# Kernel optimization log

Measured on AMD Instinct MI355X. Metric: run time of the kernel, lower is better.

Reference implementation:

```python
import jax, jax.numpy as jnp
import numpy as np
from jax.scipy.special import gammaln

T_STEPS, N_GRID, NMUL = 730, 10000, 2
NEARZERO = 1e-5
LENF = 15  # unit-hydrograph length used by UH_gamma routing
STAT_NAMES = ["parFC", "parK0", "parK1", "parK2", "parLP", "parPERC", "parUZL",
              "parTT", "parCFMAX", "parCFR", "parCWH", "parC", "parRT", "parAC"]
BOUNDS = {"parBETA": (1.0, 6.0), "parFC": (50.0, 1000.0), "parK0": (0.05, 0.9),
          "parK1": (0.01, 0.5), "parK2": (0.001, 0.2), "parLP": (0.2, 1.0),
          "parPERC": (0.0, 10.0), "parUZL": (0.0, 100.0), "parTT": (-2.5, 2.5),
          "parCFMAX": (0.5, 10.0), "parCFR": (0.0, 0.1), "parCWH": (0.0, 0.2),
          "parBETAET": (0.3, 5.0), "parC": (0.0, 1.0), "parRT": (0.0, 20.0),
          "parAC": (0.0, 2500.0)}
ROUT_A = (0.0, 2.9)
ROUT_B = (0.0, 6.5)


def _scale(p, lo, hi):
    # change_param_range: affine map of [0,1]-normalized params to physical bounds
    return p * (hi - lo) + lo


def setup_inputs() -> dict:
    key = jax.random.key(0)
    ks = jax.random.split(key, 7)
    prcp = jax.random.uniform(ks[0], (T_STEPS, N_GRID)) * 10.0          # mm/day
    tmean = jax.random.uniform(ks[1], (T_STEPS, N_GRID)) * 30.0 - 10.0  # deg C, spans parTT range
    pet = jax.random.uniform(ks[2], (T_STEPS, N_GRID)) * 5.0            # mm/day
    x_phy = jnp.stack([prcp, tmean, pet], axis=-1).astype(jnp.float32)
    ac_all = jax.random.uniform(ks[3], (N_GRID,)) * 2500.0              # drainage area per unit basin
    elev_all = jax.random.uniform(ks[4], (N_GRID,)) * 3000.0            # elevation
    params_dy = jax.random.uniform(ks[5], (T_STEPS, N_GRID, 2 * NMUL))  # dynamic: parBETA, parBETAET
    params_stat = jax.random.uniform(ks[6], (N_GRID, 14 * NMUL + 2))    # 14 static phy + 2 routing
    return {"x_phy": x_phy, "ac_all": ac_all, "elev_all": elev_all,
            "params_dy": params_dy, "params_stat": params_stat}


def _forward(x_phy, ac_all, elev_all, params_dy, params_stat):
    T, G, _ = x_phy.shape
    P, Tair, PET = x_phy[..., 0], x_phy[..., 1], x_phy[..., 2]
    # expand forcing to nmul parameter components
    Pm = jnp.broadcast_to(P[..., None], (T, G, NMUL))
    Tm = jnp.broadcast_to(Tair[..., None], (T, G, NMUL))
    PETm = jnp.broadcast_to(PET[..., None], (T, G, NMUL))
    Ac = jnp.broadcast_to(ac_all[:, None], (G, NMUL))

    # dynamic (per-timestep) params; dy_drop=0.0 -> bernoulli drop mask is all zeros,
    # so the dynamic values are used directly at every step
    dy = params_dy.reshape(T, G, 2, NMUL)
    parBETA = _scale(dy[:, :, 0], *BOUNDS["parBETA"])
    parBETAET = _scale(dy[:, :, 1], *BOUNDS["parBETAET"])

    # static params: [G, 14, NMUL]
    stat = params_stat[:, :14 * NMUL].reshape(G, 14, NMUL)
    sp = {n: _scale(stat[:, i], *BOUNDS[n]) for i, n in enumerate(STAT_NAMES)}
    rout_a = _scale(params_stat[:, 14 * NMUL], *ROUT_A)
    rout_b = _scale(params_stat[:, 14 * NMUL + 1], *ROUT_B)

    def step(carry, xt):
        SNOWPACK, MELTWATER, SM, SUZ, SLZ = carry
        Pt, Tt, PETt, beta, betaet = xt
        rain_mask = (Tt >= sp["parTT"]).astype(Pt.dtype)
        RAIN = Pt * rain_mask
        SNOW = Pt * (1.0 - rain_mask)
        # --- snow bucket ---
        SNOWPACK = SNOWPACK + SNOW
        melt = jnp.maximum(sp["parCFMAX"] * (Tt - sp["parTT"]), 0.0)
        melt = jnp.minimum(melt, SNOWPACK)
        MELTWATER = MELTWATER + melt
        SNOWPACK = SNOWPACK - melt
        refreeze = jnp.maximum(sp["parCFR"] * sp["parCFMAX"] * (sp["parTT"] - Tt), 0.0)
        refreeze = jnp.minimum(refreeze, MELTWATER)
        SNOWPACK = SNOWPACK + refreeze
        MELTWATER = MELTWATER - refreeze
        tosoil = jnp.maximum(MELTWATER - sp["parCWH"] * SNOWPACK, 0.0)
        MELTWATER = MELTWATER - tosoil
        # --- soil bucket ---
        soil_wetness = jnp.clip((SM / sp["parFC"]) ** beta, 0.0, 1.0)
        recharge = (RAIN + tosoil) * soil_wetness
        SM = SM + RAIN + tosoil - recharge
        excess = jnp.maximum(SM - sp["parFC"], 0.0)
        SM = SM - excess
        evapfactor = jnp.clip(SM / (sp["parLP"] * sp["parFC"]), 0.0, 1.0) ** betaet
        ETact = jnp.minimum(SM, PETt * evapfactor)
        SM = jnp.maximum(SM - ETact, NEARZERO)
        # capillary rise from lower groundwater zone (parC)
        capillary = jnp.minimum(SLZ, sp["parC"] * SLZ * (1.0 - jnp.minimum(SM / sp["parFC"], 1.0)))
        SM = jnp.maximum(SM + capillary, NEARZERO)
        SLZ = jnp.maximum(SLZ - capillary, NEARZERO)
        # --- groundwater buckets ---
        SUZ = SUZ + recharge + excess
        PERC = jnp.minimum(SUZ, sp["parPERC"])
        SUZ = SUZ - PERC
        Q0 = sp["parK0"] * jnp.maximum(SUZ - sp["parUZL"], 0.0)
        SUZ = SUZ - Q0
        Q1 = sp["parK1"] * SUZ
        SUZ = SUZ - Q1
        SLZ = SLZ + PERC
        # HBV 2.0 regional groundwater loss (area-dependent via parRT / parAC; reconstructed)
        gw_loss = jnp.minimum(SLZ, sp["parRT"] * jnp.clip(1.0 - Ac / (sp["parAC"] + NEARZERO), 0.0, 1.0))
        SLZ = SLZ - gw_loss
        Q2 = sp["parK2"] * SLZ
        SLZ = SLZ - Q2
        Qt = Q0 + Q1 + Q2
        return (SNOWPACK, MELTWATER, SM, SUZ, SLZ), Qt

    init = tuple(jnp.full((G, NMUL), 1e-3, dtype=x_phy.dtype) for _ in range(5))
    _, Qsimmu = jax.lax.scan(step, init, (Pm, Tm, PETm, parBETA, parBETAET))
    Qsim = Qsimmu.mean(-1)  # [T, G]; muwts=None -> uniform average over nmul components

    # --- gamma unit-hydrograph routing (UH_gamma + causal UH_conv) ---
    a = jnp.maximum(rout_a, 0.0) + 0.1       # [G]
    theta = jnp.maximum(rout_b, 0.0) + 0.5   # [G]
    t = jnp.arange(LENF, dtype=Qsim.dtype) + 0.5  # [LENF]
    w = (jnp.exp(-gammaln(a))[None, :] * theta[None, :] ** (-a[None, :])
         * t[:, None] ** (a[None, :] - 1.0) * jnp.exp(-t[:, None] / theta[None, :]))
    w = w / w.sum(0)  # [LENF, G], normalized UH weights
    # causal grouped conv: flow[t] = sum_k w[k] * Qsim[t-k]
    Qpad = jnp.pad(Qsim, ((LENF - 1, 0), (0, 0)))
    flow = jnp.zeros_like(Qsim)
    for k in range(LENF):  # fixed, small tap count
        flow = flow + w[k][None, :] * Qpad[LENF - 1 - k: LENF - 1 - k + T]
    return flow[..., None]  # [T, G, 1] routed streamflow


def reference(x_phy, ac_all, elev_all, params_dy, params_stat):
    return _forward(x_phy, ac_all, elev_all, params_dy, params_stat)
```

## Files before the change

### kernel.cpp

```cpp
#include <hip/hip_runtime.h>


#define TS 730
#define NG 10000
#define CH 15
#define NCHUNK 49
#define XSTRIDE (NG * 3)
#define DSTRIDE (NG * 4)

#define AS1 __attribute__((address_space(1)))
#define AS3 __attribute__((address_space(3)))
#define WAIT_VMCNT(n) __builtin_amdgcn_s_waitcnt(((n) & 15) | 0x70 | 0xF00 | (((n) >> 4) << 14))
#define WAIT_LGKM0    __builtin_amdgcn_s_waitcnt(0xC07F)

__device__ __forceinline__ void gload16(const float* g, float* l) {
    __builtin_amdgcn_global_load_lds((const AS1 void*)g, (AS3 void*)l, 16, 0, 0);
}
__device__ __forceinline__ float powpos(float x, float b) {
    return __builtin_amdgcn_exp2f(b * __builtin_amdgcn_logf(x));
}

__global__ __launch_bounds__(64, 1) void hbv_fused(
    const float* __restrict__ x_phy,
    const float* __restrict__ ac_all,
    const float* __restrict__ params_dy,
    const float* __restrict__ params_stat,
    float* __restrict__ out)
{
    __shared__ float xls0[1536], xls1[1536];
    __shared__ float dls0[2048], dls1[2048];

    const int lane = threadIdx.x & 63;
    const int m    = lane >> 5;
    const int cell = lane & 31;
    const int g0   = blockIdx.x * 32;
    const int g    = g0 + cell;
    const int gl   = g < NG ? g : NG - 1;
    const int g0r  = (g0 <= NG - 32) ? g0 : NG - 32;
    const int co   = cell + (g0 - g0r);
    const int cl   = co < 31 ? co : 31;

    const float* ps = params_stat + (size_t)gl * 30;
    const float FC    = ps[0  + m] * 950.f   + 50.f;
    const float K0    = ps[2  + m] * 0.85f   + 0.05f;
    const float K1    = ps[4  + m] * 0.49f   + 0.01f;
    const float K2    = ps[6  + m] * 0.199f  + 0.001f;
    const float LP    = ps[8  + m] * 0.8f    + 0.2f;
    const float PERCp = ps[10 + m] * 10.f;
    const float UZL   = ps[12 + m] * 100.f;
    const float TTp   = ps[14 + m] * 5.f     - 2.5f;
    const float CFMAX = ps[16 + m] * 9.5f    + 0.5f;
    const float CFR   = ps[18 + m] * 0.1f;
    const float CWH   = ps[20 + m] * 0.2f;
    const float Cc    = ps[22 + m];
    const float RT    = ps[24 + m] * 20.f;
    const float ACp   = ps[26 + m] * 2500.f;
    const float ra    = ps[28] * 2.9f;
    const float rb    = ps[29] * 6.5f;

    const float Acv     = ac_all[gl];
    const float invFC   = 1.f / FC;
    const float invLPFC = 1.f / (LP * FC);
    const float CFRC    = CFR * CFMAX;
    const float gwcap   = RT * fminf(fmaxf(1.f - Acv / (ACp + 1e-5f), 0.f), 1.f);

    const float a     = fmaxf(ra, 0.f) + 0.1f;
    const float th    = fmaxf(rb, 0.f) + 0.5f;
    const float am1   = a - 1.f;
    const float nl2e  = 1.44269504f / th;
    float w[CH];
    float wsum = 0.f;
#pragma unroll
    for (int k = 0; k < CH; ++k) {
        const float tk = (float)k + 0.5f;
        const float v  = __builtin_amdgcn_exp2f(am1 * __builtin_amdgcn_logf(tk) - tk * nl2e);
        w[k] = v; wsum += v;
    }
    const float wn = 0.5f / wsum;
#pragma unroll
    for (int k = 0; k < CH; ++k) w[k] *= wn;

    int offx[6], offd[8];
#pragma unroll
    for (int i = 0; i < 6; ++i) {
        int idx = i * 64 + lane;
        idx = idx < 360 ? idx : 359;
        const int row = idx / 24;
        const int col = idx - row * 24;
        offx[i] = row * XSTRIDE + col * 4;
    }
#pragma unroll
    for (int i = 0; i < 8; ++i) {
        int idx = i * 64 + lane;
        idx = idx < 480 ? idx : 479;
        const int row = idx >> 5;
        const int col = idx & 31;
        offd[i] = row * DSTRIDE + col * 4;
    }
    const float* xbase = x_phy     + (size_t)g0r * 3;
    const float* dbase = params_dy + (size_t)g0r * 4;

    auto issue = [&](int cc, float* xl, float* dl) {
        if (cc == NCHUNK - 1) {
#pragma unroll
            for (int i = 0; i < 6; ++i) {
                int idx = i * 64 + lane; idx = idx < 360 ? idx : 359;
                const int row = idx / 24, col = idx - row * 24;
                int t = cc * CH + row; t = t < TS ? t : TS - 1;
                gload16(xbase + (size_t)t * XSTRIDE + col * 4, xl + i * 256);
            }
#pragma unroll
            for (int i = 0; i < 8; ++i) {
                int idx = i * 64 + lane; idx = idx < 480 ? idx : 479;
                const int row = idx >> 5, col = idx & 31;
                int t = cc * CH + row; t = t < TS ? t : TS - 1;
                gload16(dbase + (size_t)t * DSTRIDE + col * 4, dl + i * 256);
            }
        } else {
            const float* xp = xbase + (size_t)cc * CH * XSTRIDE;
            const float* dp = dbase + (size_t)cc * CH * DSTRIDE;
#pragma unroll
            for (int i = 0; i < 6; ++i) gload16(xp + offx[i], xl + i * 256);
#pragma unroll
            for (int i = 0; i < 8; ++i) gload16(dp + offd[i], dl + i * 256);
        }
    };

    float SP = 1e-3f, MW = 1e-3f, SM = 1e-3f, SUZ = 1e-3f, SLZ = 1e-3f;
    float facc[CH];
#pragma unroll
    for (int k = 0; k < CH; ++k) facc[k] = 0.f;

    const bool doStore = (g < NG) && (lane < 32);

    auto chunk = [&](int c, const float* xl, const float* dl) {
        float ofl[CH];
        float Pc = xl[cl * 3 + 0], Tc = xl[cl * 3 + 1], Ec = xl[cl * 3 + 2];
        float4 dvc = *(const float4*)&dl[cl * 4];
#pragma unroll
        for (int j = 0; j < CH; ++j) {
            float Pn, Tn, En; float4 dvn;
            if (j < CH - 1) {
                Pn  = xl[(j + 1) * 96 + cl * 3 + 0];
                Tn  = xl[(j + 1) * 96 + cl * 3 + 1];
                En  = xl[(j + 1) * 96 + cl * 3 + 2];
                dvn = *(const float4*)&dl[(j + 1) * 128 + cl * 4];
            }
            const float Pt = Pc, Tt = Tc, PETt = Ec;
            const float beta   = (m ? dvc.y : dvc.x) * 5.f  + 1.f;
            const float betaet = (m ? dvc.w : dvc.z) * 4.7f + 0.3f;

            const float rain = (Tt >= TTp) ? Pt : 0.f;
            SP += Pt - rain;
            const float melt = fminf(fmaxf(CFMAX * (Tt - TTp), 0.f), SP);
            MW += melt; SP -= melt;
            const float refr = fminf(fmaxf(CFRC * (TTp - Tt), 0.f), MW);
            SP += refr; MW -= refr;
            const float tosoil = fmaxf(MW - CWH * SP, 0.f);
            MW -= tosoil;

            const float sw   = fminf(powpos(SM * invFC, beta), 1.f);
            const float rts  = rain + tosoil;
            SM = fmaf(rts, 1.f - sw, SM);
            const float exc = fmaxf(SM - FC, 0.f);
            SM = fminf(SM, FC);
            const float ef = powpos(fminf(SM * invLPFC, 1.f), betaet);
            const float ET = fminf(SM, PETt * ef);
            SM = fmaxf(SM - ET, 1e-5f);
            const float cap = Cc * SLZ * (1.f - fminf(SM * invFC, 1.f));
            SM  = fmaxf(SM + cap, 1e-5f);
            SLZ = fmaxf(SLZ - cap, 1e-5f);

            SUZ += rts * sw + exc;
            const float perc = fminf(SUZ, PERCp);
            SUZ -= perc;
            const float Q0 = K0 * fmaxf(SUZ - UZL, 0.f);
            SUZ -= Q0;
            const float Q1 = K1 * SUZ;
            SUZ -= Q1;
            SLZ += perc;
            const float gw = fminf(SLZ, gwcap);
            SLZ -= gw;
            const float Q2 = K2 * SLZ;
            SLZ -= Q2;
            const float Qt = Q0 + Q1 + Q2;

#pragma unroll
            for (int k = 0; k < CH; ++k)
                facc[(j + k) % CH] = fmaf(w[k], Qt, facc[(j + k) % CH]);
            ofl[j]  = facc[j];
            facc[j] = 0.f;

            Pc = Pn; Tc = Tn; Ec = En; dvc = dvn;
        }
        float prt[CH];
#pragma unroll
        for (int j = 0; j < CH; ++j) prt[j] = __shfl_xor(ofl[j], 32);
        if (doStore) {
            float* op = out + (size_t)c * CH * NG + g;
            const int tb = c * CH;
#pragma unroll
            for (int j = 0; j < CH; ++j)
                if (tb + j < TS) op[(size_t)j * NG] = ofl[j] + prt[j];
        }
    };

    issue(0, xls0, dls0);
    issue(1, xls1, dls1);

    for (int cp = 0; cp < 24; ++cp) {
        const int c0 = 2 * cp;
        WAIT_VMCNT(14);
        chunk(c0, xls0, dls0);
        WAIT_LGKM0;
        issue(c0 + 2, xls0, dls0);
        WAIT_VMCNT(14);
        chunk(c0 + 1, xls1, dls1);
        WAIT_LGKM0;
        if (cp < 23) issue(c0 + 3, xls1, dls1);
    }
    WAIT_VMCNT(14);
    chunk(48, xls0, dls0);
}

extern "C" void kernel_launch(void* const* d_in, const int* in_sizes, int n_in,
                              void* d_out, int out_size, void* d_ws, size_t ws_size,
                              hipStream_t stream) {
    const float* x_phy = (const float*)d_in[0];
    const float* ac    = (const float*)d_in[1];
    const float* pdy   = (const float*)d_in[3];
    const float* pst   = (const float*)d_in[4];
    float* out = (float*)d_out;

    const int grid = (NG + 31) / 32;
    hbv_fused<<<grid, 64, 0, stream>>>(x_phy, ac, pdy, pst, out);
}
```

Before: 323.1 us.

## Stage chunk from LDS into registers and issue next prefetch before compute

Each 15-step chunk's forcing and dynamic parameters are now read from LDS into registers up front. The global-to-LDS prefetch for chunk c+2 is issued right after that read instead of after the chunk's compute, which gives the loads more time to land. The vmcnt wait thresholds are raised so the in-flight loads and stores can overlap the compute. Some clamps also become fmed3, and the groundwater step becomes a single fmax, which shortens the serial dependence chain a little but costs more registers.

```diff
diff --git a/kernel.cpp b/kernel.cpp
--- a/kernel.cpp
+++ b/kernel.cpp
@@ -18,6 +18,9 @@
 }
 __device__ __forceinline__ float powpos(float x, float b) {
     return __builtin_amdgcn_exp2f(b * __builtin_amdgcn_logf(x));
+}
+__device__ __forceinline__ float med3(float x, float lo, float hi) {
+    return __builtin_amdgcn_fmed3f(x, lo, hi);
 }
 
 __global__ __launch_bounds__(64, 1) void hbv_fused(
@@ -133,34 +136,38 @@
 
     const bool doStore = (g < NG) && (lane < 32);
 
-    auto chunk = [&](int c, const float* xl, const float* dl) {
+    auto chunkR = [&](int c, float* xl, float* dl) {
+        float xP[CH], xT[CH], xE[CH];
+        float4 dv[CH];
+#pragma unroll
+        for (int j = 0; j < CH; ++j) {
+            xP[j] = xl[j * 96 + cl * 3 + 0];
+            xT[j] = xl[j * 96 + cl * 3 + 1];
+            xE[j] = xl[j * 96 + cl * 3 + 2];
+            dv[j] = *(const float4*)&dl[j * 128 + cl * 4];
+        }
+        WAIT_LGKM0;
+        __builtin_amdgcn_sched_barrier(0);
+        const int cn = c + 2;
+        if (cn < NCHUNK) issue(cn, xl, dl);
         float ofl[CH];
-        float Pc = xl[cl * 3 + 0], Tc = xl[cl * 3 + 1], Ec = xl[cl * 3 + 2];
-        float4 dvc = *(const float4*)&dl[cl * 4];
 #pragma unroll
         for (int j = 0; j < CH; ++j) {
-            float Pn, Tn, En; float4 dvn;
-            if (j < CH - 1) {
-                Pn  = xl[(j + 1) * 96 + cl * 3 + 0];
-                Tn  = xl[(j + 1) * 96 + cl * 3 + 1];
-                En  = xl[(j + 1) * 96 + cl * 3 + 2];
-                dvn = *(const float4*)&dl[(j + 1) * 128 + cl * 4];
-            }
-            const float Pt = Pc, Tt = Tc, PETt = Ec;
-            const float beta   = (m ? dvc.y : dvc.x) * 5.f  + 1.f;
-            const float betaet = (m ? dvc.w : dvc.z) * 4.7f + 0.3f;
+            const float Pt = xP[j], Tt = xT[j], PETt = xE[j];
+            const float beta   = (m ? dv[j].y : dv[j].x) * 5.f  + 1.f;
+            const float betaet = (m ? dv[j].w : dv[j].z) * 4.7f + 0.3f;
 
             const float rain = (Tt >= TTp) ? Pt : 0.f;
             SP += Pt - rain;
-            const float melt = fminf(fmaxf(CFMAX * (Tt - TTp), 0.f), SP);
+            const float melt = med3(CFMAX * (Tt - TTp), 0.f, SP);
             MW += melt; SP -= melt;
-            const float refr = fminf(fmaxf(CFRC * (TTp - Tt), 0.f), MW);
+            const float refr = med3(CFRC * (TTp - Tt), 0.f, MW);
             SP += refr; MW -= refr;
             const float tosoil = fmaxf(MW - CWH * SP, 0.f);
             MW -= tosoil;
 
-            const float sw   = fminf(powpos(SM * invFC, beta), 1.f);
-            const float rts  = rain + tosoil;
+            const float sw  = fminf(powpos(SM * invFC, beta), 1.f);
+            const float rts = rain + tosoil;
             SM = fmaf(rts, 1.f - sw, SM);
             const float exc = fmaxf(SM - FC, 0.f);
             SM = fminf(SM, FC);
@@ -179,8 +186,7 @@
             const float Q1 = K1 * SUZ;
             SUZ -= Q1;
             SLZ += perc;
-            const float gw = fminf(SLZ, gwcap);
-            SLZ -= gw;
+            SLZ = fmaxf(SLZ - gwcap, 0.f);
             const float Q2 = K2 * SLZ;
             SLZ -= Q2;
             const float Qt = Q0 + Q1 + Q2;
@@ -190,19 +196,18 @@
                 facc[(j + k) % CH] = fmaf(w[k], Qt, facc[(j + k) % CH]);
             ofl[j]  = facc[j];
             facc[j] = 0.f;
-
-            Pc = Pn; Tc = Tn; Ec = En; dvc = dvn;
         }
         float prt[CH];
 #pragma unroll
-        for (int j = 0; j < CH; ++j) prt[j] = __shfl_xor(ofl[j], 32);
+        for (int jj = 0; jj < CH; ++jj) prt[jj] = __shfl_xor(ofl[jj], 32);
         if (doStore) {
             float* op = out + (size_t)c * CH * NG + g;
             const int tb = c * CH;
 #pragma unroll
-            for (int j = 0; j < CH; ++j)
-                if (tb + j < TS) op[(size_t)j * NG] = ofl[j] + prt[j];
-        }
+            for (int jj = 0; jj < CH; ++jj)
+                if (tb + jj < TS) op[(size_t)jj * NG] = ofl[jj] + prt[jj];
+        }
+        __builtin_amdgcn_sched_barrier(0);
     };
 
     issue(0, xls0, dls0);
@@ -210,17 +215,13 @@
 
     for (int cp = 0; cp < 24; ++cp) {
         const int c0 = 2 * cp;
-        WAIT_VMCNT(14);
-        chunk(c0, xls0, dls0);
-        WAIT_LGKM0;
-        issue(c0 + 2, xls0, dls0);
-        WAIT_VMCNT(14);
-        chunk(c0 + 1, xls1, dls1);
-        WAIT_LGKM0;
-        if (cp < 23) issue(c0 + 3, xls1, dls1);
-    }
-    WAIT_VMCNT(14);
-    chunk(48, xls0, dls0);
+        WAIT_VMCNT(27);
+        chunkR(c0, xls0, dls0);
+        WAIT_VMCNT(27);
+        chunkR(c0 + 1, xls1, dls1);
+    }
+    WAIT_VMCNT(27);
+    chunkR(48, xls0, dls0);
 }
 
 extern "C" void kernel_launch(void* const* d_in, const int* in_sizes, int n_in,
```

Result: faster. 300.8 us (-6.9%).

## Count output stores in vmcnt waits, batch routing conv, use med3 clamps

Applied to the files above, without the earlier changes.

The vmcnt wait thresholds now include the 15 outstanding output stores per chunk, so waiting for the next chunk's LDS loads no longer also drains the stores just issued. This should let loads, stores and compute overlap more fully. The routing convolution is moved out of the per-timestep recurrence into a separate pass over buffered Qt values, which shortens the serial dependency chain. Snow clamps now use fmed3, and the groundwater loss is folded into one max. The hand-tuned wait counts depend on in-order vmcnt retirement across loads and stores, which could cause a data race if the counts are wrong.

```diff
diff --git a/kernel.cpp b/kernel.cpp
--- a/kernel.cpp
+++ b/kernel.cpp
@@ -18,6 +18,9 @@
 }
 __device__ __forceinline__ float powpos(float x, float b) {
     return __builtin_amdgcn_exp2f(b * __builtin_amdgcn_logf(x));
+}
+__device__ __forceinline__ float med3(float x, float lo, float hi) {
+    return __builtin_amdgcn_fmed3f(x, lo, hi);
 }
 
 __global__ __launch_bounds__(64, 1) void hbv_fused(
@@ -134,7 +137,7 @@
     const bool doStore = (g < NG) && (lane < 32);
 
     auto chunk = [&](int c, const float* xl, const float* dl) {
-        float ofl[CH];
+        float qts[CH];
         float Pc = xl[cl * 3 + 0], Tc = xl[cl * 3 + 1], Ec = xl[cl * 3 + 2];
         float4 dvc = *(const float4*)&dl[cl * 4];
 #pragma unroll
@@ -152,15 +155,15 @@
 
             const float rain = (Tt >= TTp) ? Pt : 0.f;
             SP += Pt - rain;
-            const float melt = fminf(fmaxf(CFMAX * (Tt - TTp), 0.f), SP);
+            const float melt = med3(CFMAX * (Tt - TTp), 0.f, SP);
             MW += melt; SP -= melt;
-            const float refr = fminf(fmaxf(CFRC * (TTp - Tt), 0.f), MW);
+            const float refr = med3(CFRC * (TTp - Tt), 0.f, MW);
             SP += refr; MW -= refr;
             const float tosoil = fmaxf(MW - CWH * SP, 0.f);
             MW -= tosoil;
 
-            const float sw   = fminf(powpos(SM * invFC, beta), 1.f);
-            const float rts  = rain + tosoil;
+            const float sw  = fminf(powpos(SM * invFC, beta), 1.f);
+            const float rts = rain + tosoil;
             SM = fmaf(rts, 1.f - sw, SM);
             const float exc = fmaxf(SM - FC, 0.f);
             SM = fminf(SM, FC);
@@ -179,47 +182,60 @@
             const float Q1 = K1 * SUZ;
             SUZ -= Q1;
             SLZ += perc;
-            const float gw = fminf(SLZ, gwcap);
-            SLZ -= gw;
+            SLZ = fmaxf(SLZ - gwcap, 0.f);
             const float Q2 = K2 * SLZ;
             SLZ -= Q2;
-            const float Qt = Q0 + Q1 + Q2;
-
+            qts[j] = Q0 + Q1 + Q2;
+
+            Pc = Pn; Tc = Tn; Ec = En; dvc = dvn;
+        }
+
+        float ofl[CH];
+#pragma unroll
+        for (int j = 0; j < CH; ++j) {
 #pragma unroll
             for (int k = 0; k < CH; ++k)
-                facc[(j + k) % CH] = fmaf(w[k], Qt, facc[(j + k) % CH]);
+                facc[(j + k) % CH] = fmaf(w[k], qts[j], facc[(j + k) % CH]);
             ofl[j]  = facc[j];
             facc[j] = 0.f;
-
-            Pc = Pn; Tc = Tn; Ec = En; dvc = dvn;
-        }
+        }
+
         float prt[CH];
 #pragma unroll
-        for (int j = 0; j < CH; ++j) prt[j] = __shfl_xor(ofl[j], 32);
+        for (int jj = 0; jj < CH; ++jj) prt[jj] = __shfl_xor(ofl[jj], 32);
         if (doStore) {
             float* op = out + (size_t)c * CH * NG + g;
             const int tb = c * CH;
 #pragma unroll
-            for (int j = 0; j < CH; ++j)
-                if (tb + j < TS) op[(size_t)j * NG] = ofl[j] + prt[j];
+            for (int jj = 0; jj < CH; ++jj)
+                if (tb + jj < TS) op[(size_t)jj * NG] = ofl[jj] + prt[jj];
         }
     };
 
     issue(0, xls0, dls0);
     issue(1, xls1, dls1);
 
-    for (int cp = 0; cp < 24; ++cp) {
+    WAIT_VMCNT(14);
+    chunk(0, xls0, dls0);
+    WAIT_LGKM0;
+    issue(2, xls0, dls0);
+    WAIT_VMCNT(29);
+    chunk(1, xls1, dls1);
+    WAIT_LGKM0;
+    issue(3, xls1, dls1);
+
+    for (int cp = 1; cp < 24; ++cp) {
         const int c0 = 2 * cp;
-        WAIT_VMCNT(14);
+        WAIT_VMCNT(29);
         chunk(c0, xls0, dls0);
         WAIT_LGKM0;
         issue(c0 + 2, xls0, dls0);
-        WAIT_VMCNT(14);
+        WAIT_VMCNT(29);
         chunk(c0 + 1, xls1, dls1);
         WAIT_LGKM0;
         if (cp < 23) issue(c0 + 3, xls1, dls1);
     }
-    WAIT_VMCNT(14);
+    WAIT_VMCNT(15);
     chunk(48, xls0, dls0);
 }
 
```

New measurement: 320.5 us. About the same (-0.8%).
